# Kernel tuning notes

Measured on AMD Instinct MI355X. Metric: run time of the kernel, lower is better.

Reference implementation:

```python
import jax, jax.numpy as jnp
import numpy as np

N_NODES = 50000
N_EDGES = 800000
HIDDEN = 128
HEADS = 4
HEAD_DIM = HIDDEN // HEADS
LAYERS = 2


def _lin(k, fan_in, fan_out):
    # xavier_uniform with gain=0.1, stored as [in, out]
    lim = 0.1 * np.sqrt(6.0 / (fan_in + fan_out))
    return jax.random.uniform(k, (fan_in, fan_out), jnp.float32, -lim, lim)


def setup_inputs() -> dict:
    key = jax.random.key(0)
    ks = jax.random.split(key, 20)
    x = jax.random.normal(ks[0], (N_NODES, HIDDEN), jnp.float32)
    edge_index = jax.random.randint(ks[1], (2, N_EDGES), 0, N_NODES, jnp.int64)
    Wi = _lin(ks[2], HIDDEN, HIDDEN); bi = jnp.zeros((HIDDEN,), jnp.float32)
    def stack(base):
        kk = jax.random.split(jax.random.fold_in(key, base), LAYERS)
        return jnp.stack([_lin(kk[l], HIDDEN, HIDDEN) for l in range(LAYERS)])
    Wq, Wk, Wv, Wo = stack(10), stack(11), stack(12), stack(13)
    bq = jnp.zeros((LAYERS, HIDDEN), jnp.float32)
    bk = jnp.zeros((LAYERS, HIDDEN), jnp.float32)
    bv = jnp.zeros((LAYERS, HIDDEN), jnp.float32)
    bo = jnp.zeros((LAYERS, HIDDEN), jnp.float32)
    kk1 = jax.random.split(jax.random.fold_in(key, 20), LAYERS)
    kk2 = jax.random.split(jax.random.fold_in(key, 21), LAYERS)
    W1 = jnp.stack([_lin(kk1[l], HIDDEN, 2 * HIDDEN) for l in range(LAYERS)])
    b1 = jnp.zeros((LAYERS, 2 * HIDDEN), jnp.float32)
    W2 = jnp.stack([_lin(kk2[l], 2 * HIDDEN, HIDDEN) for l in range(LAYERS)])
    b2 = jnp.zeros((LAYERS, HIDDEN), jnp.float32)
    return {"x": x, "edge_index": edge_index, "Wi": Wi, "bi": bi,
            "Wq": Wq, "bq": bq, "Wk": Wk, "bk": bk, "Wv": Wv, "bv": bv,
            "Wo": Wo, "bo": bo, "W1": W1, "b1": b1, "W2": W2, "b2": b2}


def _layer(x, src, dst, Wq, bq, Wk, bk, Wv, bv, Wo, bo, W1, b1, W2, b2):
    n = x.shape[0]
    residual = x
    q = (x @ Wq + bq).reshape(n, HEADS, HEAD_DIM)
    k = (x @ Wk + bk).reshape(n, HEADS, HEAD_DIM)
    v = (x @ Wv + bv).reshape(n, HEADS, HEAD_DIM)
    q_i = q[dst]            # [E, H, D]
    k_j = k[src]            # [E, H, D]
    scale = HEAD_DIM ** -0.5
    scores = jnp.einsum('ehd,ehd->eh', q_i, k_j) * scale  # [E, H]
    # NOTE: faithful to original — softmax over ALL edges (dim=0), per head
    attn = jax.nn.softmax(scores, axis=0)
    attn_out = v[src] * attn[:, :, None]  # [E, H, D]
    agg = jax.ops.segment_sum(attn_out, dst, num_segments=n)  # [N, H, D]
    out = agg.reshape(n, HIDDEN) @ Wo + bo
    x = residual + out
    residual = x
    x = jax.nn.relu(x @ W1 + b1) @ W2 + b2
    return residual + x


def reference(x, edge_index, Wi, bi, Wq, bq, Wk, bk, Wv, bv, Wo, bo, W1, b1, W2, b2):
    src, dst = edge_index[0], edge_index[1]
    x = x @ Wi + bi
    for l in range(LAYERS):
        x = _layer(x, src, dst, Wq[l], bq[l], Wk[l], bk[l], Wv[l], bv[l],
                   Wo[l], bo[l], W1[l], b1[l], W2[l], b2[l])
    return x
```

## Files before the change

kernel.cpp:

```cpp
#include <hip/hip_runtime.h>


typedef __attribute__((ext_vector_type(8))) short bf16x8;
typedef __attribute__((ext_vector_type(4))) float f32x4;

__device__ __forceinline__ unsigned short f2bf_rne(float f) {
  unsigned int u = __builtin_bit_cast(unsigned int, f);
  u = (u + 0x7fffu + ((u >> 16) & 1u)) >> 16;
  return (unsigned short)u;
}
__device__ __forceinline__ unsigned int pack2bf(float a, float b) {
  return (unsigned int)f2bf_rne(a) | ((unsigned int)f2bf_rne(b) << 16);
}
__device__ __forceinline__ float bflo(unsigned int w) {
  return __builtin_bit_cast(float, w << 16);
}
__device__ __forceinline__ float bfhi(unsigned int w) {
  return __builtin_bit_cast(float, w & 0xffff0000u);
}

template<bool RELU, bool RES, bool OUTF, bool OUTB, bool QKVH, bool AF32>
__global__ __launch_bounds__(256)
void mgemm_k(const void* __restrict__ Ain,
             const unsigned short* __restrict__ Bt,
             const float* __restrict__ bias, const float* __restrict__ R,
             float* __restrict__ Yf, unsigned short* __restrict__ Yb,
             int M, int K, int N) {
  __shared__ __align__(16) char smem[32768];
  const int t = threadIdx.x;
  const int l = t & 63;
  const int w = t >> 6, wm = w >> 1, wn = w & 1;
  const int row0 = blockIdx.x * 64;
  const int col0 = blockIdx.y * 64;

  f32x4 acc[2][2];
#pragma unroll
  for (int m = 0; m < 2; m++)
#pragma unroll
    for (int n = 0; n < 2; n++)
#pragma unroll
      for (int r = 0; r < 4; r++) acc[m][n][r] = 0.f;

  for (int kc = 0; kc < K; kc += 128) {
    if (kc) __syncthreads();
#pragma unroll
    for (int j = 0; j < 4; j++) {
      int id = j * 256 + t;
      int row = id >> 4, c16 = id & 15;
      int gr = row0 + row; if (gr >= M) gr = M - 1;
      uint4 val;
      if (AF32) {
        const float* ap = (const float*)Ain + (size_t)gr * K + kc + c16 * 8;
        float4 f0 = *(const float4*)ap;
        float4 f1 = *(const float4*)(ap + 4);
        val.x = pack2bf(f0.x, f0.y); val.y = pack2bf(f0.z, f0.w);
        val.z = pack2bf(f1.x, f1.y); val.w = pack2bf(f1.z, f1.w);
      } else {
        val = *(const uint4*)((const unsigned short*)Ain + (size_t)gr * K + kc + c16 * 8);
      }
      *(uint4*)(smem + row * 256 + ((c16 * 16) ^ ((row & 7) << 4))) = val;
    }
#pragma unroll
    for (int j = 0; j < 4; j++) {
      int id = j * 256 + t;
      int row = id >> 4, c16 = id & 15;
      uint4 val = *(const uint4*)(Bt + (size_t)(col0 + row) * K + kc + c16 * 8);
      *(uint4*)(smem + 16384 + row * 256 + ((c16 * 16) ^ ((row & 7) << 4))) = val;
    }
    __syncthreads();

#pragma unroll
    for (int ks = 0; ks < 4; ks++) {
      const int bofs = ks * 64 + (l >> 4) * 16;
      bf16x8 a[2], b[2];
#pragma unroll
      for (int m = 0; m < 2; m++) {
        int r = wm * 32 + m * 16 + (l & 15);
        a[m] = *(const bf16x8*)(smem + r * 256 + (bofs ^ ((r & 7) << 4)));
      }
#pragma unroll
      for (int n = 0; n < 2; n++) {
        int r = wn * 32 + n * 16 + (l & 15);
        b[n] = *(const bf16x8*)(smem + 16384 + r * 256 + (bofs ^ ((r & 7) << 4)));
      }
#pragma unroll
      for (int m = 0; m < 2; m++)
#pragma unroll
        for (int n = 0; n < 2; n++)
          acc[m][n] = __builtin_amdgcn_mfma_f32_16x16x32_bf16(a[m], b[n], acc[m][n], 0, 0, 0);
    }
  }

  const int rbase = row0 + wm * 32 + ((l >> 4) << 2);
  const int cl = l & 15;
#pragma unroll
  for (int n = 0; n < 2; n++) {
    int col = col0 + wn * 32 + n * 16 + cl;
    float bb = bias[col];
#pragma unroll
    for (int m = 0; m < 2; m++) {
      int rtile = rbase + m * 16;
#pragma unroll
      for (int r = 0; r < 4; r++) {
        int row = rtile + r;
        if (row < M) {
          float o = acc[m][n][r] + bb;
          if (RES) o += R[(size_t)row * N + col];
          if (RELU) o = fmaxf(o, 0.f);
          if (OUTF) Yf[(size_t)row * N + col] = o;
          if (OUTB) {
            unsigned short vb = f2bf_rne(o);
            if (QKVH) {
              if (col < 128) {
                Yb[(size_t)row * 128 + col] = vb;
              } else if (col < 256) {
                int cc = col - 128, head = cc >> 5, dd = cc & 31;
                Yb[(size_t)M * 128 + ((size_t)head * M + row) * 32 + dd] = vb;
              } else {
                Yb[(size_t)M * 256 + (size_t)row * 128 + (col - 256)] = vb;
              }
            } else {
              Yb[(size_t)row * N + col] = vb;
            }
          }
        }
      }
    }
  }
}

__global__ __launch_bounds__(256)
void prep_k(const float* __restrict__ Wi, const float* __restrict__ Wq,
            const float* __restrict__ Wk, const float* __restrict__ Wv,
            const float* __restrict__ Wo, const float* __restrict__ W1,
            const float* __restrict__ W2, const float* __restrict__ bq,
            const float* __restrict__ bk, const float* __restrict__ bv,
            unsigned short* __restrict__ WiT, unsigned short* __restrict__ WqkvT,
            unsigned short* __restrict__ WoT, unsigned short* __restrict__ W1T,
            unsigned short* __restrict__ W2T, float* __restrict__ bqkv) {
  int o = blockIdx.x * 256 + threadIdx.x;
  if (o < 16384) {
    int n = o >> 7, k = o & 127;
    WiT[o] = f2bf_rne(Wi[k * 128 + n]);
    return;
  }
  o -= 16384;
  if (o < 98304) {
    int seg = o >> 15; int r = o & 32767;
    int l = r >> 14; int rr = r & 16383;
    int n = rr >> 7, k = rr & 127;
    const float* W = (seg == 0) ? Wq : (seg == 1) ? Wk : Wv;
    WqkvT[(size_t)l * 49152 + seg * 16384 + n * 128 + k] =
        f2bf_rne(W[(size_t)l * 16384 + k * 128 + n]);
    return;
  }
  o -= 98304;
  if (o < 32768) {
    int l = o >> 14; int rr = o & 16383;
    int n = rr >> 7, k = rr & 127;
    WoT[(size_t)l * 16384 + n * 128 + k] = f2bf_rne(Wo[(size_t)l * 16384 + k * 128 + n]);
    return;
  }
  o -= 32768;
  if (o < 65536) {
    int l = o >> 15; int rr = o & 32767;
    int n = rr >> 7, k = rr & 127;
    W1T[(size_t)l * 32768 + n * 128 + k] = f2bf_rne(W1[(size_t)l * 32768 + k * 256 + n]);
    return;
  }
  o -= 65536;
  if (o < 65536) {
    int l = o >> 15; int rr = o & 32767;
    int n = rr >> 8, k = rr & 255;
    W2T[(size_t)l * 32768 + n * 256 + k] = f2bf_rne(W2[(size_t)l * 32768 + k * 128 + n]);
    return;
  }
  o -= 65536;
  if (o < 768) {
    int l = o / 384, c = o - l * 384;
    float v = (c < 128) ? bq[l * 128 + c] : (c < 256) ? bk[l * 128 + c - 128] : bv[l * 128 + c - 256];
    bqkv[o] = v;
  }
}

__global__ __launch_bounds__(256)
void rs_hist8_k(const int* __restrict__ key, int* __restrict__ gh,
                int E, int shift, int nblk) {
  __shared__ int h[256];
  int t = threadIdx.x, b = blockIdx.x;
  h[t] = 0;
  __syncthreads();
#pragma unroll
  for (int j = 0; j < 8; j++) {
    int i = b * 2048 + j * 256 + t;
    if (i < E) atomicAdd(&h[(key[i] >> shift) & 255], 1);
  }
  __syncthreads();
  gh[t * nblk + b] = h[t];
}

__global__ __launch_bounds__(256)
void scanA_k(const int* __restrict__ a, int* __restrict__ bsum, int n) {
  __shared__ int sm[256];
  int b = blockIdx.x, t = threadIdx.x;
  int base = b * 2048 + t * 8;
  int s = 0;
#pragma unroll
  for (int j = 0; j < 8; j++) {
    int i = base + j;
    if (i < n) s += a[i];
  }
  sm[t] = s; __syncthreads();
  for (int d = 128; d >= 1; d >>= 1) {
    if (t < d) sm[t] += sm[t + d];
    __syncthreads();
  }
  if (t == 0) bsum[b] = sm[0];
}

__global__ __launch_bounds__(64)
void scanB_k(int* __restrict__ bsum, int nb) {
  if (threadIdx.x == 0 && blockIdx.x == 0) {
    int run = 0;
    for (int b = 0; b < nb; b++) { int v = bsum[b]; bsum[b] = run; run += v; }
  }
}

__global__ __launch_bounds__(256)
void scanC_k(int* __restrict__ a, const int* __restrict__ bsum, int n) {
  __shared__ int sm[256];
  int b = blockIdx.x, t = threadIdx.x;
  int base = b * 2048 + t * 8;
  int vals[8];
  int s = 0;
#pragma unroll
  for (int j = 0; j < 8; j++) {
    int i = base + j;
    vals[j] = (i < n) ? a[i] : 0;
    s += vals[j];
  }
  sm[t] = s; __syncthreads();
  for (int d = 1; d < 256; d <<= 1) {
    int v = (t >= d) ? sm[t - d] : 0;
    __syncthreads();
    sm[t] += v;
    __syncthreads();
  }
  int run = bsum[b] + sm[t] - s;
#pragma unroll
  for (int j = 0; j < 8; j++) {
    int i = base + j;
    if (i < n) { a[i] = run; run += vals[j]; }
  }
}

__global__ __launch_bounds__(256)
void rs_scatter8_k(const int* __restrict__ keyIn, const int* __restrict__ payIn,
                   int* __restrict__ keyOut, int* __restrict__ payOut,
                   const int* __restrict__ gh, int E, int shift, int nblk) {
  __shared__ int base[256];
  __shared__ int wcnt[4][256];
  int t = threadIdx.x, b = blockIdx.x;
  int w = t >> 6, ln = t & 63;
  unsigned long long lmask = (1ull << ln) - 1ull;
  base[t] = gh[t * nblk + b];
  wcnt[0][t] = 0; wcnt[1][t] = 0; wcnt[2][t] = 0; wcnt[3][t] = 0;
  __syncthreads();
  for (int j = 0; j < 8; j++) {
    int i = b * 2048 + j * 256 + t;
    bool valid = i < E;
    int kv = valid ? keyIn[i] : 0;
    int d = (kv >> shift) & 255;
    if (valid) atomicAdd(&wcnt[w][d], 1);
    unsigned long long mm = __ballot(valid);
#pragma unroll
    for (int bit = 0; bit < 8; bit++) {
      unsigned long long bb = __ballot((d >> bit) & 1);
      mm &= ((d >> bit) & 1) ? bb : ~bb;
    }
    int myrank = __popcll(mm & lmask);
    __syncthreads();
    if (valid) {
      int wbase = 0;
      for (int w2 = 0; w2 < w; w2++) wbase += wcnt[w2][d];
      int pos = base[d] + wbase + myrank;
      keyOut[pos] = kv;
      payOut[pos] = payIn ? payIn[i] : i;
    }
    __syncthreads();
    base[t] += wcnt[0][t] + wcnt[1][t] + wcnt[2][t] + wcnt[3][t];
    wcnt[0][t] = 0; wcnt[1][t] = 0; wcnt[2][t] = 0; wcnt[3][t] = 0;
    __syncthreads();
  }
}

__global__ __launch_bounds__(256)
void boundsmeta_k(const int* __restrict__ key, const int* __restrict__ pay,
                  const int* __restrict__ src, int* __restrict__ off,
                  int* __restrict__ srcP, int E, int N) {
  int i = blockIdx.x * 256 + threadIdx.x;
  if (i >= E) return;
  srcP[i] = src[pay[i]];
  int k1 = key[i];
  int k0 = (i == 0) ? -1 : key[i - 1];
  for (int d = k0 + 1; d <= k1; d++) off[d] = i;
  if (i == E - 1) {
    for (int d = k1 + 1; d <= N; d++) off[d] = E;
  }
}

__global__ __launch_bounds__(256)
void scores_k(const unsigned short* __restrict__ QKV,
              const int* __restrict__ srcP, const int* __restrict__ dstP,
              float* __restrict__ Sp, float* __restrict__ psum,
              int E, int Nn, float scale, int nb) {
  __shared__ float sm[256];
  int t = threadIdx.x, h = blockIdx.y;
  int i = blockIdx.x * 256 + t;
  float ex = 0.f;
  if (i < E) {
    const uint4* qp = (const uint4*)(QKV + (size_t)dstP[i] * 128 + h * 32);
    const uint4* kp = (const uint4*)(QKV + (size_t)Nn * 128 + ((size_t)h * Nn + srcP[i]) * 32);
    float acc = 0.f;
#pragma unroll
    for (int j = 0; j < 4; j++) {
      uint4 q4 = qp[j], k4 = kp[j];
      acc += bflo(q4.x) * bflo(k4.x) + bfhi(q4.x) * bfhi(k4.x);
      acc += bflo(q4.y) * bflo(k4.y) + bfhi(q4.y) * bfhi(k4.y);
      acc += bflo(q4.z) * bflo(k4.z) + bfhi(q4.z) * bfhi(k4.z);
      acc += bflo(q4.w) * bflo(k4.w) + bfhi(q4.w) * bfhi(k4.w);
    }
    ex = expf(acc * scale);
    Sp[(size_t)h * E + i] = ex;
  }
  sm[t] = ex; __syncthreads();
  for (int s = 128; s >= 1; s >>= 1) {
    if (t < s) sm[t] += sm[t + s];
    __syncthreads();
  }
  if (t == 0) psum[h * nb + blockIdx.x] = sm[0];
}

__global__ __launch_bounds__(256)
void reduceIz_k(const float* __restrict__ psum, float* __restrict__ iz, int nb) {
  __shared__ float sm[256];
  int h = blockIdx.x, t = threadIdx.x;
  float a = 0.f;
  for (int j = t; j < nb; j += 256) a += psum[(size_t)h * nb + j];
  sm[t] = a; __syncthreads();
  for (int s = 128; s >= 1; s >>= 1) {
    if (t < s) sm[t] += sm[t + s];
    __syncthreads();
  }
  if (t == 0) iz[h] = 1.0f / sm[0];
}

__global__ __launch_bounds__(256)
void gatheragg_k(const float* __restrict__ Sp, const float* __restrict__ iz,
                 const unsigned short* __restrict__ QKV,
                 const int* __restrict__ srcP, const int* __restrict__ off,
                 unsigned short* __restrict__ AGb, int Nn, int E) {
  int node = blockIdx.x * 4 + (threadIdx.x >> 6);
  if (node >= Nn) return;
  int l = threadIdx.x & 63;
  int p = l >> 5;
  int q = l & 31;
  int h = q >> 3;
  const unsigned short* Vb = QKV + (size_t)Nn * 256 + q * 4;
  const float* Sph = Sp + (size_t)h * E;
  float izh = iz[h];
  int lo = off[node], hi = off[node + 1];
  float a0 = 0.f, a1 = 0.f, a2 = 0.f, a3 = 0.f;
  int i = lo + p;
  for (; i + 6 < hi; i += 8) {
    int s0 = srcP[i], s1 = srcP[i + 2], s2 = srcP[i + 4], s3 = srcP[i + 6];
    float c0 = Sph[i] * izh, c1 = Sph[i + 2] * izh;
    float c2 = Sph[i + 4] * izh, c3 = Sph[i + 6] * izh;
    uint2 v0 = *(const uint2*)(Vb + (size_t)s0 * 128);
    uint2 v1 = *(const uint2*)(Vb + (size_t)s1 * 128);
    uint2 v2 = *(const uint2*)(Vb + (size_t)s2 * 128);
    uint2 v3 = *(const uint2*)(Vb + (size_t)s3 * 128);
    a0 = fmaf(c0, bflo(v0.x), a0); a1 = fmaf(c0, bfhi(v0.x), a1);
    a2 = fmaf(c0, bflo(v0.y), a2); a3 = fmaf(c0, bfhi(v0.y), a3);
    a0 = fmaf(c1, bflo(v1.x), a0); a1 = fmaf(c1, bfhi(v1.x), a1);
    a2 = fmaf(c1, bflo(v1.y), a2); a3 = fmaf(c1, bfhi(v1.y), a3);
    a0 = fmaf(c2, bflo(v2.x), a0); a1 = fmaf(c2, bfhi(v2.x), a1);
    a2 = fmaf(c2, bflo(v2.y), a2); a3 = fmaf(c2, bfhi(v2.y), a3);
    a0 = fmaf(c3, bflo(v3.x), a0); a1 = fmaf(c3, bfhi(v3.x), a1);
    a2 = fmaf(c3, bflo(v3.y), a2); a3 = fmaf(c3, bfhi(v3.y), a3);
  }
  for (; i < hi; i += 2) {
    int s = srcP[i];
    float c = Sph[i] * izh;
    uint2 v = *(const uint2*)(Vb + (size_t)s * 128);
    a0 = fmaf(c, bflo(v.x), a0); a1 = fmaf(c, bfhi(v.x), a1);
    a2 = fmaf(c, bflo(v.y), a2); a3 = fmaf(c, bfhi(v.y), a3);
  }
  a0 += __shfl_down(a0, 32); a1 += __shfl_down(a1, 32);
  a2 += __shfl_down(a2, 32); a3 += __shfl_down(a3, 32);
  if (p == 0) {
    uint2 out;
    out.x = pack2bf(a0, a1);
    out.y = pack2bf(a2, a3);
    *(uint2*)(AGb + (size_t)node * 128 + q * 4) = out;
  }
}

extern "C" void kernel_launch(void* const* d_in, const int* in_sizes, int n_in,
                              void* d_out, int out_size, void* d_ws, size_t ws_size,
                              hipStream_t stream) {
  const float* x_in = (const float*)d_in[0];
  const int*   ei   = (const int*)d_in[1];
  const float* Wi = (const float*)d_in[2];
  const float* bi = (const float*)d_in[3];
  const float* Wq = (const float*)d_in[4];  const float* bq = (const float*)d_in[5];
  const float* Wk = (const float*)d_in[6];  const float* bk = (const float*)d_in[7];
  const float* Wv = (const float*)d_in[8];  const float* bv = (const float*)d_in[9];
  const float* Wo = (const float*)d_in[10]; const float* bo = (const float*)d_in[11];
  const float* W1 = (const float*)d_in[12]; const float* b1 = (const float*)d_in[13];
  const float* W2 = (const float*)d_in[14]; const float* b2 = (const float*)d_in[15];

  const int N = in_sizes[0] / 128;
  const int E = in_sizes[1] / 2;
  const int* src = ei;
  const int* dst = ei + E;

  char* w = (char*)d_ws;
  auto alloc = [&](size_t bytes) -> char* {
    char* p = w;
    w += (bytes + 255) & ~(size_t)255;
    return p;
  };
  float*          X    = (float*)alloc((size_t)N * 128 * 4);
  unsigned short* Xb   = (unsigned short*)alloc((size_t)N * 128 * 2);
  unsigned short* QKVb = (unsigned short*)alloc((size_t)N * 384 * 2);
  unsigned short* Hb   = QKVb;
  unsigned short* AGb  = (unsigned short*)alloc((size_t)N * 128 * 2);
  float*          Sp   = (float*)alloc((size_t)E * 4 * 4);
  const int nb = (E + 255) / 256;
  float* psum = (float*)alloc((size_t)4 * nb * 4);
  float* iz   = (float*)alloc(16);
  unsigned short* WiT   = (unsigned short*)alloc(16384 * 2);
  unsigned short* WqkvT = (unsigned short*)alloc((size_t)2 * 384 * 128 * 2);
  unsigned short* WoT   = (unsigned short*)alloc((size_t)2 * 16384 * 2);
  unsigned short* W1T   = (unsigned short*)alloc((size_t)2 * 32768 * 2);
  unsigned short* W2T   = (unsigned short*)alloc((size_t)2 * 32768 * 2);
  float* bqkv = (float*)alloc(768 * 4);
  int* off  = (int*)alloc((size_t)(N + 1) * 4);
  int* kA   = (int*)alloc((size_t)E * 4);
  int* pA   = (int*)alloc((size_t)E * 4);
  int* kB   = (int*)alloc((size_t)E * 4);
  int* pB   = (int*)alloc((size_t)E * 4);
  int* srcP = (int*)alloc((size_t)E * 4);
  const int nblk = (E + 2047) / 2048;
  const int ghn  = 256 * nblk;
  int* gh   = (int*)alloc((size_t)ghn * 4);
  int* bsum = (int*)alloc(256 * 4);

  const float scale = 0.17677669529663687f;
  dim3 blk(256);
  const int gx = (N + 63) / 64;
  dim3 gP(gx, 2), gQKV(gx, 6), gW1(gx, 4);
  const int gEe = (E + 255) / 256;
  const int nsb = (ghn + 2047) / 2048;
  dim3 gSc(nb, 4);
  const int gAgg = (N + 3) / 4;

  rs_hist8_k<<<nblk, blk, 0, stream>>>(dst, gh, E, 0, nblk);
  scanA_k<<<nsb, blk, 0, stream>>>(gh, bsum, ghn);
  scanB_k<<<1, 64, 0, stream>>>(bsum, nsb);
  scanC_k<<<nsb, blk, 0, stream>>>(gh, bsum, ghn);
  rs_scatter8_k<<<nblk, blk, 0, stream>>>(dst, nullptr, kA, pA, gh, E, 0, nblk);
  rs_hist8_k<<<nblk, blk, 0, stream>>>(kA, gh, E, 8, nblk);
  scanA_k<<<nsb, blk, 0, stream>>>(gh, bsum, ghn);
  scanB_k<<<1, 64, 0, stream>>>(bsum, nsb);
  scanC_k<<<nsb, blk, 0, stream>>>(gh, bsum, ghn);
  rs_scatter8_k<<<nblk, blk, 0, stream>>>(kA, pA, kB, pB, gh, E, 8, nblk);
  boundsmeta_k<<<gEe, blk, 0, stream>>>(kB, pB, src, off, srcP, E, N);
  int* dstP = kB;

  prep_k<<<1091, blk, 0, stream>>>(Wi, Wq, Wk, Wv, Wo, W1, W2, bq, bk, bv,
                                   WiT, WqkvT, WoT, W1T, W2T, bqkv);

  mgemm_k<false, false, true, true, false, true><<<gP, blk, 0, stream>>>(
      x_in, WiT, bi, nullptr, X, Xb, N, 128, 128);

  for (int l = 0; l < 2; l++) {
    const float* bo_l = bo + l * 128;
    const float* b1_l = b1 + l * 256;
    const float* b2_l = b2 + l * 128;

    mgemm_k<false, false, false, true, true, false><<<gQKV, blk, 0, stream>>>(
        Xb, WqkvT + (size_t)l * 384 * 128, bqkv + l * 384, nullptr, nullptr, QKVb, N, 128, 384);

    scores_k<<<gSc, blk, 0, stream>>>(QKVb, srcP, dstP, Sp, psum, E, N, scale, nb);
    reduceIz_k<<<4, blk, 0, stream>>>(psum, iz, nb);

    gatheragg_k<<<gAgg, blk, 0, stream>>>(Sp, iz, QKVb, srcP, off, AGb, N, E);

    mgemm_k<false, true, true, true, false, false><<<gP, blk, 0, stream>>>(
        AGb, WoT + (size_t)l * 16384, bo_l, X, X, Xb, N, 128, 128);
    mgemm_k<true, false, false, true, false, false><<<gW1, blk, 0, stream>>>(
        Xb, W1T + (size_t)l * 32768, b1_l, nullptr, nullptr, Hb, N, 128, 256);
    if (l == 0) {
      mgemm_k<false, true, true, true, false, false><<<gP, blk, 0, stream>>>(
          Hb, W2T + (size_t)l * 32768, b2_l, X, X, Xb, N, 256, 128);
    } else {
      mgemm_k<false, true, true, false, false, false><<<gP, blk, 0, stream>>>(
          Hb, W2T + (size_t)l * 32768, b2_l, X, (float*)d_out, nullptr, N, 256, 128);
    }
  }
}
```

Measured before the change: 428.8 us.

## Fuse edge scores, exp and aggregation into one per-node kernel, defer softmax normalization

Replaces the separate scores kernel (writing per-edge exp values) and the gather-aggregate kernel with one dst-sorted per-node kernel. It computes q·k, exp and the weighted V sum in one pass, and emits per-block partial sums for the global softmax denominator. Normalization by 1/Z moves into the Wo GEMM's A-load as a per-head scale, and the QKV output changes to a plain row-major [N,384] layout. This removes the E×4 score buffer round trip and one launch. In exchange the unnormalized aggregate is stored in fp32 (twice the bytes of bf16), and K/V gathers now stride 384-element rows.

```diff
diff --git a/kernel.cpp b/kernel.cpp
--- a/kernel.cpp
+++ b/kernel.cpp
@@ -19,11 +19,12 @@
   return __builtin_bit_cast(float, w & 0xffff0000u);
 }
 
-template<bool RELU, bool RES, bool OUTF, bool OUTB, bool QKVH, bool AF32>
+template<bool RELU, bool RES, bool OUTF, bool OUTB, bool AF32, bool SCALE>
 __global__ __launch_bounds__(256)
 void mgemm_k(const void* __restrict__ Ain,
              const unsigned short* __restrict__ Bt,
              const float* __restrict__ bias, const float* __restrict__ R,
+             const float* __restrict__ scl,
              float* __restrict__ Yf, unsigned short* __restrict__ Yb,
              int M, int K, int N) {
   __shared__ __align__(16) char smem[32768];
@@ -53,8 +54,9 @@
         const float* ap = (const float*)Ain + (size_t)gr * K + kc + c16 * 8;
         float4 f0 = *(const float4*)ap;
         float4 f1 = *(const float4*)(ap + 4);
-        val.x = pack2bf(f0.x, f0.y); val.y = pack2bf(f0.z, f0.w);
-        val.z = pack2bf(f1.x, f1.y); val.w = pack2bf(f1.z, f1.w);
+        float s = SCALE ? scl[(kc + c16 * 8) >> 5] : 1.f;
+        val.x = pack2bf(f0.x * s, f0.y * s); val.y = pack2bf(f0.z * s, f0.w * s);
+        val.z = pack2bf(f1.x * s, f1.y * s); val.w = pack2bf(f1.z * s, f1.w * s);
       } else {
         val = *(const uint4*)((const unsigned short*)Ain + (size_t)gr * K + kc + c16 * 8);
       }
@@ -108,21 +110,7 @@
           if (RES) o += R[(size_t)row * N + col];
           if (RELU) o = fmaxf(o, 0.f);
           if (OUTF) Yf[(size_t)row * N + col] = o;
-          if (OUTB) {
-            unsigned short vb = f2bf_rne(o);
-            if (QKVH) {
-              if (col < 128) {
-                Yb[(size_t)row * 128 + col] = vb;
-              } else if (col < 256) {
-                int cc = col - 128, head = cc >> 5, dd = cc & 31;
-                Yb[(size_t)M * 128 + ((size_t)head * M + row) * 32 + dd] = vb;
-              } else {
-                Yb[(size_t)M * 256 + (size_t)row * 128 + (col - 256)] = vb;
-              }
-            } else {
-              Yb[(size_t)row * N + col] = vb;
-            }
-          }
+          if (OUTB) Yb[(size_t)row * N + col] = f2bf_rne(o);
         }
       }
     }
@@ -310,35 +298,68 @@
 }
 
 __global__ __launch_bounds__(256)
-void scores_k(const unsigned short* __restrict__ QKV,
-              const int* __restrict__ srcP, const int* __restrict__ dstP,
-              float* __restrict__ Sp, float* __restrict__ psum,
-              int E, int Nn, float scale, int nb) {
-  __shared__ float sm[256];
-  int t = threadIdx.x, h = blockIdx.y;
-  int i = blockIdx.x * 256 + t;
-  float ex = 0.f;
-  if (i < E) {
-    const uint4* qp = (const uint4*)(QKV + (size_t)dstP[i] * 128 + h * 32);
-    const uint4* kp = (const uint4*)(QKV + (size_t)Nn * 128 + ((size_t)h * Nn + srcP[i]) * 32);
-    float acc = 0.f;
-#pragma unroll
-    for (int j = 0; j < 4; j++) {
-      uint4 q4 = qp[j], k4 = kp[j];
-      acc += bflo(q4.x) * bflo(k4.x) + bfhi(q4.x) * bfhi(k4.x);
-      acc += bflo(q4.y) * bflo(k4.y) + bfhi(q4.y) * bfhi(k4.y);
-      acc += bflo(q4.z) * bflo(k4.z) + bfhi(q4.z) * bfhi(k4.z);
-      acc += bflo(q4.w) * bflo(k4.w) + bfhi(q4.w) * bfhi(k4.w);
-    }
-    ex = expf(acc * scale);
-    Sp[(size_t)h * E + i] = ex;
-  }
-  sm[t] = ex; __syncthreads();
-  for (int s = 128; s >= 1; s >>= 1) {
-    if (t < s) sm[t] += sm[t + s];
-    __syncthreads();
-  }
-  if (t == 0) psum[h * nb + blockIdx.x] = sm[0];
+void edgefuse_k(const unsigned short* __restrict__ QKV,
+                const int* __restrict__ srcP, const int* __restrict__ off,
+                float* __restrict__ AGu, float* __restrict__ psum,
+                int Nn, float scale) {
+  __shared__ float ps[4][4];
+  int t = threadIdx.x;
+  int wv = t >> 6, l = t & 63;
+  int p = l >> 5, q = l & 31, h = q >> 3;
+  int node = blockIdx.x * 4 + wv;
+  float a0 = 0.f, a1 = 0.f, a2 = 0.f, a3 = 0.f;
+  float pacc = 0.f;
+  if (node < Nn) {
+    uint2 qv = *(const uint2*)(QKV + (size_t)node * 384 + q * 4);
+    int lo = off[node], hi = off[node + 1];
+    int i = lo + p;
+    for (; i + 2 < hi; i += 4) {
+      int s0 = srcP[i], s1 = srcP[i + 2];
+      const unsigned short* r0 = QKV + (size_t)s0 * 384;
+      const unsigned short* r1 = QKV + (size_t)s1 * 384;
+      uint2 k0 = *(const uint2*)(r0 + 128 + q * 4);
+      uint2 k1 = *(const uint2*)(r1 + 128 + q * 4);
+      uint2 v0 = *(const uint2*)(r0 + 256 + q * 4);
+      uint2 v1 = *(const uint2*)(r1 + 256 + q * 4);
+      float d0 = bflo(qv.x) * bflo(k0.x) + bfhi(qv.x) * bfhi(k0.x)
+               + bflo(qv.y) * bflo(k0.y) + bfhi(qv.y) * bfhi(k0.y);
+      float d1 = bflo(qv.x) * bflo(k1.x) + bfhi(qv.x) * bfhi(k1.x)
+               + bflo(qv.y) * bflo(k1.y) + bfhi(qv.y) * bfhi(k1.y);
+      d0 += __shfl_xor(d0, 1); d0 += __shfl_xor(d0, 2); d0 += __shfl_xor(d0, 4);
+      d1 += __shfl_xor(d1, 1); d1 += __shfl_xor(d1, 2); d1 += __shfl_xor(d1, 4);
+      float c0 = expf(d0 * scale);
+      float c1 = expf(d1 * scale);
+      if ((q & 7) == 0) pacc += c0 + c1;
+      a0 = fmaf(c0, bflo(v0.x), a0); a1 = fmaf(c0, bfhi(v0.x), a1);
+      a2 = fmaf(c0, bflo(v0.y), a2); a3 = fmaf(c0, bfhi(v0.y), a3);
+      a0 = fmaf(c1, bflo(v1.x), a0); a1 = fmaf(c1, bfhi(v1.x), a1);
+      a2 = fmaf(c1, bflo(v1.y), a2); a3 = fmaf(c1, bfhi(v1.y), a3);
+    }
+    if (i < hi) {
+      int s = srcP[i];
+      const unsigned short* r = QKV + (size_t)s * 384;
+      uint2 kf = *(const uint2*)(r + 128 + q * 4);
+      uint2 vf = *(const uint2*)(r + 256 + q * 4);
+      float d = bflo(qv.x) * bflo(kf.x) + bfhi(qv.x) * bfhi(kf.x)
+              + bflo(qv.y) * bflo(kf.y) + bfhi(qv.y) * bfhi(kf.y);
+      d += __shfl_xor(d, 1); d += __shfl_xor(d, 2); d += __shfl_xor(d, 4);
+      float c = expf(d * scale);
+      if ((q & 7) == 0) pacc += c;
+      a0 = fmaf(c, bflo(vf.x), a0); a1 = fmaf(c, bfhi(vf.x), a1);
+      a2 = fmaf(c, bflo(vf.y), a2); a3 = fmaf(c, bfhi(vf.y), a3);
+    }
+  }
+  a0 += __shfl_down(a0, 32); a1 += __shfl_down(a1, 32);
+  a2 += __shfl_down(a2, 32); a3 += __shfl_down(a3, 32);
+  pacc += __shfl_down(pacc, 32);
+  if (p == 0 && (q & 7) == 0) ps[wv][h] = pacc;
+  __syncthreads();
+  if (t < 4) psum[(size_t)t * gridDim.x + blockIdx.x] =
+      ps[0][t] + ps[1][t] + ps[2][t] + ps[3][t];
+  if (node < Nn && p == 0) {
+    float4 o = make_float4(a0, a1, a2, a3);
+    *(float4*)(AGu + (size_t)node * 128 + q * 4) = o;
+  }
 }
 
 __global__ __launch_bounds__(256)
@@ -353,57 +374,6 @@
     __syncthreads();
   }
   if (t == 0) iz[h] = 1.0f / sm[0];
-}
-
-__global__ __launch_bounds__(256)
-void gatheragg_k(const float* __restrict__ Sp, const float* __restrict__ iz,
-                 const unsigned short* __restrict__ QKV,
-                 const int* __restrict__ srcP, const int* __restrict__ off,
-                 unsigned short* __restrict__ AGb, int Nn, int E) {
-  int node = blockIdx.x * 4 + (threadIdx.x >> 6);
-  if (node >= Nn) return;
-  int l = threadIdx.x & 63;
-  int p = l >> 5;
-  int q = l & 31;
-  int h = q >> 3;
-  const unsigned short* Vb = QKV + (size_t)Nn * 256 + q * 4;
-  const float* Sph = Sp + (size_t)h * E;
-  float izh = iz[h];
-  int lo = off[node], hi = off[node + 1];
-  float a0 = 0.f, a1 = 0.f, a2 = 0.f, a3 = 0.f;
-  int i = lo + p;
-  for (; i + 6 < hi; i += 8) {
-    int s0 = srcP[i], s1 = srcP[i + 2], s2 = srcP[i + 4], s3 = srcP[i + 6];
-    float c0 = Sph[i] * izh, c1 = Sph[i + 2] * izh;
-    float c2 = Sph[i + 4] * izh, c3 = Sph[i + 6] * izh;
-    uint2 v0 = *(const uint2*)(Vb + (size_t)s0 * 128);
-    uint2 v1 = *(const uint2*)(Vb + (size_t)s1 * 128);
-    uint2 v2 = *(const uint2*)(Vb + (size_t)s2 * 128);
-    uint2 v3 = *(const uint2*)(Vb + (size_t)s3 * 128);
-    a0 = fmaf(c0, bflo(v0.x), a0); a1 = fmaf(c0, bfhi(v0.x), a1);
-    a2 = fmaf(c0, bflo(v0.y), a2); a3 = fmaf(c0, bfhi(v0.y), a3);
-    a0 = fmaf(c1, bflo(v1.x), a0); a1 = fmaf(c1, bfhi(v1.x), a1);
-    a2 = fmaf(c1, bflo(v1.y), a2); a3 = fmaf(c1, bfhi(v1.y), a3);
-    a0 = fmaf(c2, bflo(v2.x), a0); a1 = fmaf(c2, bfhi(v2.x), a1);
-    a2 = fmaf(c2, bflo(v2.y), a2); a3 = fmaf(c2, bfhi(v2.y), a3);
-    a0 = fmaf(c3, bflo(v3.x), a0); a1 = fmaf(c3, bfhi(v3.x), a1);
-    a2 = fmaf(c3, bflo(v3.y), a2); a3 = fmaf(c3, bfhi(v3.y), a3);
-  }
-  for (; i < hi; i += 2) {
-    int s = srcP[i];
-    float c = Sph[i] * izh;
-    uint2 v = *(const uint2*)(Vb + (size_t)s * 128);
-    a0 = fmaf(c, bflo(v.x), a0); a1 = fmaf(c, bfhi(v.x), a1);
-    a2 = fmaf(c, bflo(v.y), a2); a3 = fmaf(c, bfhi(v.y), a3);
-  }
-  a0 += __shfl_down(a0, 32); a1 += __shfl_down(a1, 32);
-  a2 += __shfl_down(a2, 32); a3 += __shfl_down(a3, 32);
-  if (p == 0) {
-    uint2 out;
-    out.x = pack2bf(a0, a1);
-    out.y = pack2bf(a2, a3);
-    *(uint2*)(AGb + (size_t)node * 128 + q * 4) = out;
-  }
 }
 
 extern "C" void kernel_launch(void* const* d_in, const int* in_sizes, int n_in,
@@ -435,10 +405,9 @@
   unsigned short* Xb   = (unsigned short*)alloc((size_t)N * 128 * 2);
   unsigned short* QKVb = (unsigned short*)alloc((size_t)N * 384 * 2);
   unsigned short* Hb   = QKVb;
-  unsigned short* AGb  = (unsigned short*)alloc((size_t)N * 128 * 2);
-  float*          Sp   = (float*)alloc((size_t)E * 4 * 4);
-  const int nb = (E + 255) / 256;
-  float* psum = (float*)alloc((size_t)4 * nb * 4);
+  float*          AGu  = (float*)alloc((size_t)N * 128 * 4);
+  const int nbS = (N + 3) / 4;
+  float* psum = (float*)alloc((size_t)4 * nbS * 4);
   float* iz   = (float*)alloc(16);
   unsigned short* WiT   = (unsigned short*)alloc(16384 * 2);
   unsigned short* WqkvT = (unsigned short*)alloc((size_t)2 * 384 * 128 * 2);
@@ -463,8 +432,6 @@
   dim3 gP(gx, 2), gQKV(gx, 6), gW1(gx, 4);
   const int gEe = (E + 255) / 256;
   const int nsb = (ghn + 2047) / 2048;
-  dim3 gSc(nb, 4);
-  const int gAgg = (N + 3) / 4;
 
   rs_hist8_k<<<nblk, blk, 0, stream>>>(dst, gh, E, 0, nblk);
   scanA_k<<<nsb, blk, 0, stream>>>(gh, bsum, ghn);
@@ -477,37 +444,35 @@
   scanC_k<<<nsb, blk, 0, stream>>>(gh, bsum, ghn);
   rs_scatter8_k<<<nblk, blk, 0, stream>>>(kA, pA, kB, pB, gh, E, 8, nblk);
   boundsmeta_k<<<gEe, blk, 0, stream>>>(kB, pB, src, off, srcP, E, N);
-  int* dstP = kB;
 
   prep_k<<<1091, blk, 0, stream>>>(Wi, Wq, Wk, Wv, Wo, W1, W2, bq, bk, bv,
                                    WiT, WqkvT, WoT, W1T, W2T, bqkv);
 
-  mgemm_k<false, false, true, true, false, true><<<gP, blk, 0, stream>>>(
-      x_in, WiT, bi, nullptr, X, Xb, N, 128, 128);
+  mgemm_k<false, false, true, true, true, false><<<gP, blk, 0, stream>>>(
+      x_in, WiT, bi, nullptr, nullptr, X, Xb, N, 128, 128);
 
   for (int l = 0; l < 2; l++) {
     const float* bo_l = bo + l * 128;
     const float* b1_l = b1 + l * 256;
     const float* b2_l = b2 + l * 128;
 
-    mgemm_k<false, false, false, true, true, false><<<gQKV, blk, 0, stream>>>(
-        Xb, WqkvT + (size_t)l * 384 * 128, bqkv + l * 384, nullptr, nullptr, QKVb, N, 128, 384);
-
-    scores_k<<<gSc, blk, 0, stream>>>(QKVb, srcP, dstP, Sp, psum, E, N, scale, nb);
-    reduceIz_k<<<4, blk, 0, stream>>>(psum, iz, nb);
-
-    gatheragg_k<<<gAgg, blk, 0, stream>>>(Sp, iz, QKVb, srcP, off, AGb, N, E);
-
-    mgemm_k<false, true, true, true, false, false><<<gP, blk, 0, stream>>>(
-        AGb, WoT + (size_t)l * 16384, bo_l, X, X, Xb, N, 128, 128);
+    mgemm_k<false, false, false, true, false, false><<<gQKV, blk, 0, stream>>>(
+        Xb, WqkvT + (size_t)l * 384 * 128, bqkv + l * 384, nullptr, nullptr,
+        nullptr, QKVb, N, 128, 384);
+
+    edgefuse_k<<<nbS, blk, 0, stream>>>(QKVb, srcP, off, AGu, psum, N, scale);
+    reduceIz_k<<<4, blk, 0, stream>>>(psum, iz, nbS);
+
+    mgemm_k<false, true, true, true, true, true><<<gP, blk, 0, stream>>>(
+        AGu, WoT + (size_t)l * 16384, bo_l, X, iz, X, Xb, N, 128, 128);
     mgemm_k<true, false, false, true, false, false><<<gW1, blk, 0, stream>>>(
-        Xb, W1T + (size_t)l * 32768, b1_l, nullptr, nullptr, Hb, N, 128, 256);
+        Xb, W1T + (size_t)l * 32768, b1_l, nullptr, nullptr, nullptr, Hb, N, 128, 256);
     if (l == 0) {
       mgemm_k<false, true, true, true, false, false><<<gP, blk, 0, stream>>>(
-          Hb, W2T + (size_t)l * 32768, b2_l, X, X, Xb, N, 256, 128);
+          Hb, W2T + (size_t)l * 32768, b2_l, X, nullptr, X, Xb, N, 256, 128);
     } else {
       mgemm_k<false, true, true, false, false, false><<<gP, blk, 0, stream>>>(
-          Hb, W2T + (size_t)l * 32768, b2_l, X, (float*)d_out, nullptr, N, 256, 128);
-    }
-  }
-}
+          Hb, W2T + (size_t)l * 32768, b2_l, X, nullptr, (float*)d_out, nullptr, N, 256, 128);
+    }
+  }
+}
```

Result: no change. 430.8 us (+0.5%).
